# Optimization experiments

Measured on AMD Instinct MI355X. Metric: run time of the kernel, lower is better.

The kernel has to match this reference:

```python
import jax, jax.numpy as jnp
import numpy as np

N = 100000      # nodes
E = 1600000     # edges (avg degree 16)
IN = 128        # input feature dim
H = 64          # hidden size (= per-head out_channels, heads=1)
EMB = 16        # event embedding size
NEG_SLOPE = 0.2


def setup_inputs() -> dict:
    key = jax.random.key(0)
    ks = jax.random.split(key, 20)
    rn = lambda k, shape, s=0.05: jax.random.normal(k, shape, dtype=jnp.float32) * s
    inp = {
        "x": jax.random.normal(ks[0], (N, IN), dtype=jnp.float32),
        "edge_index": jax.random.randint(ks[1], (2, E), 0, N),
        "h_prev1": jax.random.normal(ks[2], (N, H), dtype=jnp.float32),
        "h_prev2": jax.random.normal(ks[3], (N, H), dtype=jnp.float32),
        # SparseGATConv params (heads=1)
        "W_gat": rn(ks[4], (H, IN)),
        "attn_l": rn(ks[5], (H,)),
        "attn_r": rn(ks[6], (H,)),
        "b_gat": jnp.zeros((H,), jnp.float32),
        # MinGRU 1
        "Wz1": rn(ks[7], (H, H)), "bz1": jnp.zeros((H,), jnp.float32),
        "Wh1": rn(ks[8], (H, H)), "bh1": jnp.zeros((H,), jnp.float32),
        # MinGRU 2
        "Wz2": rn(ks[9], (H, H)), "bz2": jnp.zeros((H,), jnp.float32),
        "Wh2": rn(ks[10], (H, H)), "bh2": jnp.zeros((H,), jnp.float32),
        # event heads
        "We1": rn(ks[11], (EMB, H)), "be1": jnp.zeros((EMB,), jnp.float32),
        "We2": rn(ks[12], (EMB, H)), "be2": jnp.zeros((EMB,), jnp.float32),
        "We3": rn(ks[13], (EMB, H)), "be3": jnp.zeros((EMB,), jnp.float32),
        # time prediction head
        "Wfc": rn(ks[14], (1, H)), "bfc": jnp.zeros((1,), jnp.float32),
    }
    return inp


def _min_gru(x, h_prev, Wz, bz, Wh, bh):
    z = jax.nn.sigmoid(x @ Wz.T + bz)
    h_tilde = jnp.tanh(x @ Wh.T + bh)
    return (1.0 - z) * h_prev + z * h_tilde


def reference(x, edge_index, h_prev1, h_prev2,
              W_gat, attn_l, attn_r, b_gat,
              Wz1, bz1, Wh1, bh1, Wz2, bz2, Wh2, bh2,
              We1, be1, We2, be2, We3, be3, Wfc, bfc):
    src, dst = edge_index[0], edge_index[1]
    # --- SparseGATConv (heads=1, concat -> [N, H]) ---
    h = x @ W_gat.T                      # [N, H]
    a1 = h @ attn_l                      # [N]  (sum over out_channels)
    a2 = h @ attn_r                      # [N]
    e = a1[src] + a2[dst]                # [E]  edge scores
    e = jnp.where(e > 0, e, NEG_SLOPE * e)  # leaky relu
    # segment softmax over incoming edges of each dst (numerically stable)
    m = jax.lax.stop_gradient(jax.ops.segment_max(e, dst, num_segments=N))
    ex = jnp.exp(e - m[dst])
    denom = jax.ops.segment_sum(ex, dst, num_segments=N)
    alpha = ex / denom[dst]              # [E]
    # dropout on alpha skipped (eval mode)
    msg = h[src] * alpha[:, None]        # [E, H]
    out = jax.ops.segment_sum(msg, dst, num_segments=N) + b_gat  # [N, H]
    # proj = Identity (gat_heads == 1)
    h1 = _min_gru(out, h_prev1, Wz1, bz1, Wh1, bh1)
    h2 = _min_gru(h1, h_prev2, Wz2, bz2, Wh2, bh2)
    c1 = h2 @ We1.T + be1
    c2 = h2 @ We2.T + be2
    c3 = h2 @ We3.T + be3
    candidate_events = jnp.stack([c1, c2, c3], axis=1)  # [N, 3, EMB]
    time_prediction = (h2 @ Wfc.T + bfc)[:, 0]          # [N]
    return candidate_events, time_prediction
```

## Files before the change

### kernel.cpp

```cpp
#include <hip/hip_runtime.h>

#define NN 100000
#define NE 1600000
#define HF 64

#define CHUNK 8192
#define NCH   196
#define NBKT  512
#define BSH   8
#define BNODES 256
#define MAXBE 5120

__device__ __forceinline__ unsigned short f2bf(float f) {
  unsigned int u = __float_as_uint(f);
  unsigned int r = (u + 0x7FFFu + ((u >> 16) & 1u)) >> 16;
  return (unsigned short)r;
}
__device__ __forceinline__ float bf2f(unsigned short s) {
  return __uint_as_float(((unsigned int)s) << 16);
}

__global__ __launch_bounds__(256) void k1_gemm_x(
    const float* __restrict__ x, const float* __restrict__ Wg,
    const float* __restrict__ attn_l, const float* __restrict__ attn_r,
    unsigned short* __restrict__ h, float* __restrict__ a1, float* __restrict__ a2)
{
  __shared__ float xa[64 * 128];
  __shared__ float wb[64 * 128];
  const int t = threadIdx.x;
  const int nbase = blockIdx.x * 64;
  const float4* Wg4 = (const float4*)Wg;
  const float4* x4  = (const float4*)x;
  float4* xa4 = (float4*)xa;
  float4* wb4 = (float4*)wb;
#pragma unroll
  for (int it = 0; it < 8; ++it) {
    int g = t + it * 256;
    int r = g >> 5, c = g & 31;
    wb4[r * 32 + (c ^ ((r >> 2) & 15))] = Wg4[g];
  }
#pragma unroll
  for (int it = 0; it < 8; ++it) {
    int g = t + it * 256;
    int r = g >> 5, c = g & 31;
    int node = nbase + r;
    float4 v = make_float4(0.f, 0.f, 0.f, 0.f);
    if (node < NN) v = x4[(size_t)node * 32 + c];
    xa4[r * 32 + (c ^ ((r >> 2) & 15))] = v;
  }
  __syncthreads();
  const int jg = t & 15, ng = t >> 4;
  const int j0 = jg * 4, n0 = ng * 4;
  float acc[4][4] = {};
#pragma unroll 8
  for (int kc = 0; kc < 32; ++kc) {
    float4 a[4], b[4];
#pragma unroll
    for (int i = 0; i < 4; ++i) a[i] = xa4[(n0 + i) * 32 + (kc ^ ng)];
#pragma unroll
    for (int j = 0; j < 4; ++j) b[j] = wb4[(j0 + j) * 32 + (kc ^ jg)];
#pragma unroll
    for (int i = 0; i < 4; ++i)
#pragma unroll
      for (int j = 0; j < 4; ++j)
        acc[i][j] += a[i].x * b[j].x + a[i].y * b[j].y + a[i].z * b[j].z + a[i].w * b[j].w;
  }
  float al[4], ar[4];
#pragma unroll
  for (int j = 0; j < 4; ++j) { al[j] = attn_l[j0 + j]; ar[j] = attn_r[j0 + j]; }
#pragma unroll
  for (int i = 0; i < 4; ++i) {
    int node = nbase + n0 + i;
    float p1 = acc[i][0]*al[0] + acc[i][1]*al[1] + acc[i][2]*al[2] + acc[i][3]*al[3];
    float p2 = acc[i][0]*ar[0] + acc[i][1]*ar[1] + acc[i][2]*ar[2] + acc[i][3]*ar[3];
#pragma unroll
    for (int m = 1; m < 16; m <<= 1) { p1 += __shfl_xor(p1, m); p2 += __shfl_xor(p2, m); }
    if (node < NN) {
      ushort4 hb;
      hb.x = f2bf(acc[i][0]); hb.y = f2bf(acc[i][1]);
      hb.z = f2bf(acc[i][2]); hb.w = f2bf(acc[i][3]);
      *(ushort4*)&h[(size_t)node * 64 + j0] = hb;
      if (jg == 0) { a1[node] = p1; a2[node] = p2; }
    }
  }
}

__global__ __launch_bounds__(256) void p1_hist(const int* __restrict__ dst,
                                               int* __restrict__ hist_blk)
{
  __shared__ int hl[NBKT];
  const int t = threadIdx.x, blk = blockIdx.x;
  for (int b = t; b < NBKT; b += 256) hl[b] = 0;
  __syncthreads();
  const int e0 = blk * CHUNK;
  const int n = min(CHUNK, NE - e0);
  for (int i = t * 4; i < n; i += 1024) {
    int4 d = *(const int4*)&dst[e0 + i];
    atomicAdd(&hl[d.x >> BSH], 1);
    atomicAdd(&hl[d.y >> BSH], 1);
    atomicAdd(&hl[d.z >> BSH], 1);
    atomicAdd(&hl[d.w >> BSH], 1);
  }
  __syncthreads();
  for (int b = t; b < NBKT; b += 256) hist_blk[blk * NBKT + b] = hl[b];
}

__global__ __launch_bounds__(256) void p2a_colscan(int* __restrict__ hist_blk,
                                                   int* __restrict__ btot)
{
  __shared__ int s[256];
  const int b = blockIdx.x, t = threadIdx.x;
  int v = (t < NCH) ? hist_blk[t * NBKT + b] : 0;
  s[t] = v;
  __syncthreads();
  for (int off = 1; off < 256; off <<= 1) {
    int add = (t >= off) ? s[t - off] : 0;
    __syncthreads();
    s[t] += add;
    __syncthreads();
  }
  if (t < NCH) hist_blk[t * NBKT + b] = s[t] - v;
  if (t == 255) btot[b] = s[255];
}

__global__ __launch_bounds__(512) void p2b_scan(const int* __restrict__ btot,
                                                int* __restrict__ bstart)
{
  __shared__ int s[512];
  const int t = threadIdx.x;
  int v = btot[t];
  s[t] = v;
  __syncthreads();
  for (int off = 1; off < 512; off <<= 1) {
    int add = (t >= off) ? s[t - off] : 0;
    __syncthreads();
    s[t] += add;
    __syncthreads();
  }
  bstart[t] = s[t] - v;
  if (t == 511) bstart[512] = s[511];
}

__global__ __launch_bounds__(256) void p3_scatter(
    const int* __restrict__ src, const int* __restrict__ dst,
    const int* __restrict__ hist_blk, const int* __restrict__ bstart,
    int2* __restrict__ part)
{
  __shared__ int hl[NBKT];
  __shared__ int loff[NBKT];
  __shared__ int cur[NBKT];
  __shared__ int sb[NBKT];
  __shared__ int q[256];
  __shared__ int2 buf[CHUNK];
  const int t = threadIdx.x, blk = blockIdx.x;
  const int e0 = blk * CHUNK;
  const int n = min(CHUNK, NE - e0);
  for (int b = t; b < NBKT; b += 256) hl[b] = 0;
  __syncthreads();
  for (int i = t * 4; i < n; i += 1024) {
    int4 d = *(const int4*)&dst[e0 + i];
    atomicAdd(&hl[d.x >> BSH], 1);
    atomicAdd(&hl[d.y >> BSH], 1);
    atomicAdd(&hl[d.z >> BSH], 1);
    atomicAdd(&hl[d.w >> BSH], 1);
  }
  __syncthreads();
  int va = hl[2 * t], vb = hl[2 * t + 1];
  int pr = va + vb;
  q[t] = pr;
  __syncthreads();
  for (int off = 1; off < 256; off <<= 1) {
    int add = (t >= off) ? q[t - off] : 0;
    __syncthreads();
    q[t] += add;
    __syncthreads();
  }
  int qe = q[t] - pr;
  loff[2 * t] = qe;       loff[2 * t + 1] = qe + va;
  cur[2 * t]  = qe;       cur[2 * t + 1]  = qe + va;
  sb[2 * t]     = bstart[2 * t]     + hist_blk[blk * NBKT + 2 * t];
  sb[2 * t + 1] = bstart[2 * t + 1] + hist_blk[blk * NBKT + 2 * t + 1];
  __syncthreads();
  for (int i = t; i < n; i += 256) {
    int s = src[e0 + i], d = dst[e0 + i];
    int p = atomicAdd(&cur[d >> BSH], 1);
    buf[p] = make_int2(s, d);
  }
  __syncthreads();
  for (int i = t; i < n; i += 256) {
    int2 e = buf[i];
    int bk = e.y >> BSH;
    part[sb[bk] + (i - loff[bk])] = e;
  }
}

__global__ __launch_bounds__(256) void p4_csr(
    const int2* __restrict__ part, const int* __restrict__ bstart,
    int* __restrict__ srcs, int* __restrict__ rs, int* __restrict__ cnt)
{
  __shared__ int cl[BNODES];
  __shared__ int s[256];
  __shared__ int rsl[BNODES];
  __shared__ int curl[BNODES];
  __shared__ int2 eb[MAXBE];
  __shared__ int osrc[MAXBE];
  const int b = blockIdx.x, t = threadIdx.x;
  const int e0 = bstart[b];
  int n = bstart[b + 1] - e0;
  if (n > MAXBE) n = MAXBE;
  cl[t] = 0;
  __syncthreads();
  for (int i = t; i < n; i += 256) {
    int2 e = part[e0 + i];
    eb[i] = e;
    atomicAdd(&cl[e.y & (BNODES - 1)], 1);
  }
  __syncthreads();
  int v = cl[t];
  s[t] = v;
  __syncthreads();
  for (int off = 1; off < 256; off <<= 1) {
    int add = (t >= off) ? s[t - off] : 0;
    __syncthreads();
    s[t] += add;
    __syncthreads();
  }
  rsl[t] = s[t] - v;
  curl[t] = s[t] - v;
  __syncthreads();
  for (int i = t; i < n; i += 256) {
    int2 e = eb[i];
    int p = atomicAdd(&curl[e.y & (BNODES - 1)], 1);
    osrc[p] = e.x;
  }
  __syncthreads();
  for (int i = t; i < n; i += 256) srcs[e0 + i] = osrc[i];
  const int node = b * BNODES + t;
  if (node < NN) { rs[node] = e0 + rsl[t]; cnt[node] = v; }
}

__global__ __launch_bounds__(256) void k5_aggregate(
    const int* __restrict__ srcs, const int* __restrict__ row_start,
    const int* __restrict__ cnt,
    const float* __restrict__ a1, const float* __restrict__ a2,
    const unsigned short* __restrict__ h, const float* __restrict__ b_gat,
    float* __restrict__ outw)
{
  const int wid  = (blockIdx.x * 256 + threadIdx.x) >> 6;
  const int lane = threadIdx.x & 63;
  if (wid >= NN) return;
  const int r0  = row_start[wid];
  const int deg = cnt[wid];
  const float a2v = a2[wid];
  const int fq = (lane & 15) * 4;
  const int eg = lane >> 4;
  float dsum = 0.f;
  float acc[4] = {0.f, 0.f, 0.f, 0.f};
  for (int base = 0; base < deg; base += 64) {
    int i = base + lane;
    int s = 0; float ex = 0.f;
    if (i < deg) {
      s = srcs[r0 + i];
      float sc = a1[s] + a2v;
      sc = sc > 0.f ? sc : 0.2f * sc;
      ex = __expf(sc);
    }
    dsum += ex;
    int nv = min(64, deg - base);
    for (int c = 0; c < nv; c += 16) {
      int se[4]; float ae[4];
#pragma unroll
      for (int u = 0; u < 4; ++u) {
        int idx = c + u * 4 + eg;
        se[u] = __shfl(s, idx);
        ae[u] = __shfl(ex, idx);
      }
      ushort4 hv[4];
#pragma unroll
      for (int u = 0; u < 4; ++u)
        hv[u] = *(const ushort4*)&h[(size_t)se[u] * 64 + fq];
#pragma unroll
      for (int u = 0; u < 4; ++u) {
        acc[0] = fmaf(ae[u], bf2f(hv[u].x), acc[0]);
        acc[1] = fmaf(ae[u], bf2f(hv[u].y), acc[1]);
        acc[2] = fmaf(ae[u], bf2f(hv[u].z), acc[2]);
        acc[3] = fmaf(ae[u], bf2f(hv[u].w), acc[3]);
      }
    }
  }
#pragma unroll
  for (int m = 1; m < 64; m <<= 1) dsum += __shfl_xor(dsum, m);
  const float inv = (deg > 0) ? 1.0f / dsum : 0.f;
#pragma unroll
  for (int k = 0; k < 4; ++k) {
    acc[k] += __shfl_xor(acc[k], 16);
    acc[k] += __shfl_xor(acc[k], 32);
  }
  if (lane < 16) {
    float4 bg = *(const float4*)&b_gat[fq];
    float4 o;
    o.x = acc[0] * inv + bg.x;
    o.y = acc[1] * inv + bg.y;
    o.z = acc[2] * inv + bg.z;
    o.w = acc[3] * inv + bg.w;
    *(float4*)&outw[(size_t)wid * 64 + fq] = o;
  }
}

__device__ __forceinline__ void stage_w64(float* dst, const float* src, int t)
{
  const float4* s4 = (const float4*)src;
  float4* d4 = (float4*)dst;
#pragma unroll
  for (int it = 0; it < 4; ++it) {
    int g = t + it * 256;
    int r = g >> 4, c = g & 15;
    d4[r * 16 + (c ^ ((r >> 2) & 15))] = s4[g];
  }
}

__device__ __forceinline__ void gemm64_acc(
    const float* at, const float* bw,
    int n0, int j0, int ng, int jg, float acc[4][4])
{
  const float4* a4 = (const float4*)at;
  const float4* b4 = (const float4*)bw;
#pragma unroll 4
  for (int kc = 0; kc < 16; ++kc) {
    float4 a[4], p[4];
#pragma unroll
    for (int i = 0; i < 4; ++i) a[i] = a4[(n0 + i) * 16 + (kc ^ ng)];
#pragma unroll
    for (int j = 0; j < 4; ++j) p[j] = b4[(j0 + j) * 16 + (kc ^ jg)];
#pragma unroll
    for (int i = 0; i < 4; ++i)
#pragma unroll
      for (int j = 0; j < 4; ++j)
        acc[i][j] += a[i].x*p[j].x + a[i].y*p[j].y + a[i].z*p[j].z + a[i].w*p[j].w;
  }
}

__device__ __forceinline__ void gru_phase(
    const float* at, const float* wz_lds, const float* wh_lds,
    const float* __restrict__ bz, const float* __restrict__ bh,
    const float* __restrict__ hp,
    int nbase, int n0, int j0, int ng, int jg, float hout[4][4])
{
  float zz[4][4];
  {
    float acc[4][4] = {};
    gemm64_acc(at, wz_lds, n0, j0, ng, jg, acc);
#pragma unroll
    for (int i = 0; i < 4; ++i)
#pragma unroll
      for (int j = 0; j < 4; ++j)
        zz[i][j] = 1.f / (1.f + __expf(-(acc[i][j] + bz[j0 + j])));
  }
  {
    float acc[4][4] = {};
    gemm64_acc(at, wh_lds, n0, j0, ng, jg, acc);
#pragma unroll
    for (int i = 0; i < 4; ++i) {
      int node = nbase + n0 + i;
      float4 hp4 = make_float4(0.f, 0.f, 0.f, 0.f);
      if (node < NN) hp4 = *(const float4*)&hp[(size_t)node * 64 + j0];
      float hpv[4] = {hp4.x, hp4.y, hp4.z, hp4.w};
#pragma unroll
      for (int j = 0; j < 4; ++j) {
        float ht = tanhf(acc[i][j] + bh[j0 + j]);
        hout[i][j] = (1.f - zz[i][j]) * hpv[j] + zz[i][j] * ht;
      }
    }
  }
}

__global__ __launch_bounds__(256) void k6_gru_heads(
    const float* __restrict__ outw,
    const float* __restrict__ hp1, const float* __restrict__ hp2,
    const float* __restrict__ Wz1, const float* __restrict__ bz1,
    const float* __restrict__ Wh1, const float* __restrict__ bh1,
    const float* __restrict__ Wz2, const float* __restrict__ bz2,
    const float* __restrict__ Wh2, const float* __restrict__ bh2,
    const float* __restrict__ We1, const float* __restrict__ We2,
    const float* __restrict__ We3, const float* __restrict__ Wfc,
    const float* __restrict__ be1, const float* __restrict__ be2,
    const float* __restrict__ be3, const float* __restrict__ bfc,
    float* __restrict__ cand, float* __restrict__ tpred)
{
  __shared__ float at[64 * 64];
  __shared__ float b1[64 * 64];
  __shared__ float b2[64 * 64];
  const int t = threadIdx.x;
  const int nbase = blockIdx.x * 64;
  const int jg = t & 15, ng = t >> 4;
  const int j0 = jg * 4, n0 = ng * 4;
  float4* at4 = (float4*)at;

  {
    const float4* o4 = (const float4*)outw;
#pragma unroll
    for (int it = 0; it < 4; ++it) {
      int g = t + it * 256;
      int r = g >> 4, c = g & 15;
      int node = nbase + r;
      float4 v = make_float4(0.f, 0.f, 0.f, 0.f);
      if (node < NN) v = o4[(size_t)node * 16 + c];
      at4[r * 16 + (c ^ ((r >> 2) & 15))] = v;
    }
  }
  stage_w64(b1, Wz1, t);
  stage_w64(b2, Wh1, t);
  __syncthreads();

  float h1v[4][4];
  gru_phase(at, b1, b2, bz1, bh1, hp1, nbase, n0, j0, ng, jg, h1v);
  __syncthreads();
#pragma unroll
  for (int i = 0; i < 4; ++i)
    at4[(n0 + i) * 16 + (jg ^ ng)] = make_float4(h1v[i][0], h1v[i][1], h1v[i][2], h1v[i][3]);
  stage_w64(b1, Wz2, t);
  stage_w64(b2, Wh2, t);
  __syncthreads();

  float h2v[4][4];
  gru_phase(at, b1, b2, bz2, bh2, hp2, nbase, n0, j0, ng, jg, h2v);
  __syncthreads();
#pragma unroll
  for (int i = 0; i < 4; ++i)
    at4[(n0 + i) * 16 + (jg ^ ng)] = make_float4(h2v[i][0], h2v[i][1], h2v[i][2], h2v[i][3]);
  {
    float4* b14 = (float4*)b1;
#pragma unroll
    for (int it = 0; it < 4; ++it) {
      int g = t + it * 256;
      int r = g >> 4, c = g & 15;
      float4 v = make_float4(0.f, 0.f, 0.f, 0.f);
      if (g < 256)       v = ((const float4*)We1)[g];
      else if (g < 512)  v = ((const float4*)We2)[g - 256];
      else if (g < 768)  v = ((const float4*)We3)[g - 512];
      else if (g < 784)  v = ((const float4*)Wfc)[g - 768];
      b14[r * 16 + (c ^ ((r >> 2) & 15))] = v;
    }
  }
  __syncthreads();

  float acc3[4][4] = {};
  gemm64_acc(at, b1, n0, j0, ng, jg, acc3);
  float bias[4];
#pragma unroll
  for (int j = 0; j < 4; ++j) {
    int jj = j0 + j;
    bias[j] = (jj < 16) ? be1[jj]
            : (jj < 32) ? be2[jj - 16]
            : (jj < 48) ? be3[jj - 32]
            : (jj == 48) ? bfc[0] : 0.f;
  }
#pragma unroll
  for (int i = 0; i < 4; ++i) {
    int node = nbase + n0 + i;
    if (node >= NN) continue;
    if (j0 < 48) {
      *(float4*)&cand[(size_t)node * 48 + j0] =
          make_float4(acc3[i][0] + bias[0], acc3[i][1] + bias[1],
                      acc3[i][2] + bias[2], acc3[i][3] + bias[3]);
    } else if (j0 == 48) {
      tpred[node] = acc3[i][0] + bias[0];
    }
  }
}

extern "C" void kernel_launch(void* const* d_in, const int* in_sizes, int n_in,
                              void* d_out, int out_size, void* d_ws, size_t ws_size,
                              hipStream_t stream)
{
  (void)in_sizes; (void)n_in; (void)out_size; (void)ws_size;
  const float* x      = (const float*)d_in[0];
  const int*   ei     = (const int*)  d_in[1];
  const float* hp1    = (const float*)d_in[2];
  const float* hp2    = (const float*)d_in[3];
  const float* Wg     = (const float*)d_in[4];
  const float* attn_l = (const float*)d_in[5];
  const float* attn_r = (const float*)d_in[6];
  const float* b_gat  = (const float*)d_in[7];
  const float* Wz1    = (const float*)d_in[8];
  const float* bz1    = (const float*)d_in[9];
  const float* Wh1    = (const float*)d_in[10];
  const float* bh1    = (const float*)d_in[11];
  const float* Wz2    = (const float*)d_in[12];
  const float* bz2    = (const float*)d_in[13];
  const float* Wh2    = (const float*)d_in[14];
  const float* bh2    = (const float*)d_in[15];
  const float* We1    = (const float*)d_in[16];
  const float* be1    = (const float*)d_in[17];
  const float* We2    = (const float*)d_in[18];
  const float* be2    = (const float*)d_in[19];
  const float* We3    = (const float*)d_in[20];
  const float* be3    = (const float*)d_in[21];
  const float* Wfc    = (const float*)d_in[22];
  const float* bfc    = (const float*)d_in[23];

  const int* srcp = ei;
  const int* dstp = ei + NE;

  char* ws = (char*)d_ws;
  unsigned short* h = (unsigned short*)(ws + 0);
  float* a1       = (float*)(ws + 12800000);
  float* a2       = (float*)(ws + 13200000);
  int*   hist_blk = (int*)  (ws + 13600000);
  int*   btot     = (int*)  (ws + 14010000);
  int*   bstart   = (int*)  (ws + 14020000);
  int*   rs       = (int*)  (ws + 14030000);
  int*   cnt      = (int*)  (ws + 14430000);
  int*   srcs     = (int*)  (ws + 14830000);
  int2*  part     = (int2*) (ws + 21230000);
  float* outw     = (float*)(ws + 21230000);

  float* cand = (float*)d_out;
  float* tp   = cand + (size_t)NN * 48;

  k1_gemm_x<<<(NN + 63) / 64, 256, 0, stream>>>(x, Wg, attn_l, attn_r, h, a1, a2);
  p1_hist<<<NCH, 256, 0, stream>>>(dstp, hist_blk);
  p2a_colscan<<<NBKT, 256, 0, stream>>>(hist_blk, btot);
  p2b_scan<<<1, 512, 0, stream>>>(btot, bstart);
  p3_scatter<<<NCH, 256, 0, stream>>>(srcp, dstp, hist_blk, bstart, part);
  p4_csr<<<(NN + BNODES - 1) / BNODES, 256, 0, stream>>>(part, bstart, srcs, rs, cnt);
  k5_aggregate<<<(NN * 64 + 255) / 256, 256, 0, stream>>>(srcs, rs, cnt, a1, a2, h, b_gat, outw);
  k6_gru_heads<<<(NN + 63) / 64, 256, 0, stream>>>(outw, hp1, hp2,
      Wz1, bz1, Wh1, bh1, Wz2, bz2, Wh2, bh2,
      We1, We2, We3, Wfc, be1, be2, be3, bfc, cand, tp);
}
```

Measured before the change: 384.1 us.

## Use bf16 MFMA for GRU and head GEMMs with bf16 aggregate output

Replaces the fp32 scalar-FMA 64x64 GEMMs in the GRU/heads kernel with bf16 MFMA 16x16x32 instructions. A small prep kernel converts and packs the weights to bf16 beforehand. The aggregation kernel now writes its output in bf16, which halves that intermediate's traffic. This trades precision on the GRU inputs and hidden states for matrix-core throughput, and adds one extra launch.

```diff
diff --git a/kernel.cpp b/kernel.cpp
--- a/kernel.cpp
+++ b/kernel.cpp
@@ -11,6 +11,9 @@
 #define BNODES 256
 #define MAXBE 5120
 
+typedef __attribute__((ext_vector_type(8))) short bf16x8;
+typedef __attribute__((ext_vector_type(4))) float f32x4;
+
 __device__ __forceinline__ unsigned short f2bf(float f) {
   unsigned int u = __float_as_uint(f);
   unsigned int r = (u + 0x7FFFu + ((u >> 16) & 1u)) >> 16;
@@ -18,6 +21,31 @@
 }
 __device__ __forceinline__ float bf2f(unsigned short s) {
   return __uint_as_float(((unsigned int)s) << 16);
+}
+
+__global__ __launch_bounds__(256) void k0_prep(
+    const float* __restrict__ Wz1, const float* __restrict__ Wh1,
+    const float* __restrict__ Wz2, const float* __restrict__ Wh2,
+    const float* __restrict__ We1, const float* __restrict__ We2,
+    const float* __restrict__ We3, const float* __restrict__ Wfc,
+    unsigned short* __restrict__ wbf)
+{
+  int idx = blockIdx.x * 256 + threadIdx.x;
+  if (idx >= 5 * 4096) return;
+  int m = idx >> 12, e = idx & 4095;
+  float v = 0.f;
+  if (m == 0) v = Wz1[e];
+  else if (m == 1) v = Wh1[e];
+  else if (m == 2) v = Wz2[e];
+  else if (m == 3) v = Wh2[e];
+  else {
+    int row = e >> 6, k = e & 63;
+    if (row < 16)      v = We1[row * 64 + k];
+    else if (row < 32) v = We2[(row - 16) * 64 + k];
+    else if (row < 48) v = We3[(row - 32) * 64 + k];
+    else if (row == 48) v = Wfc[k];
+  }
+  wbf[idx] = f2bf(v);
 }
 
 __global__ __launch_bounds__(256) void k1_gemm_x(
@@ -244,7 +272,7 @@
     const int* __restrict__ cnt,
     const float* __restrict__ a1, const float* __restrict__ a2,
     const unsigned short* __restrict__ h, const float* __restrict__ b_gat,
-    float* __restrict__ outw)
+    unsigned short* __restrict__ outw)
 {
   const int wid  = (blockIdx.x * 256 + threadIdx.x) >> 6;
   const int lane = threadIdx.x & 63;
@@ -298,173 +326,152 @@
   }
   if (lane < 16) {
     float4 bg = *(const float4*)&b_gat[fq];
-    float4 o;
-    o.x = acc[0] * inv + bg.x;
-    o.y = acc[1] * inv + bg.y;
-    o.z = acc[2] * inv + bg.z;
-    o.w = acc[3] * inv + bg.w;
-    *(float4*)&outw[(size_t)wid * 64 + fq] = o;
-  }
-}
-
-__device__ __forceinline__ void stage_w64(float* dst, const float* src, int t)
-{
-  const float4* s4 = (const float4*)src;
-  float4* d4 = (float4*)dst;
-#pragma unroll
-  for (int it = 0; it < 4; ++it) {
+    ushort4 o;
+    o.x = f2bf(acc[0] * inv + bg.x);
+    o.y = f2bf(acc[1] * inv + bg.y);
+    o.z = f2bf(acc[2] * inv + bg.z);
+    o.w = f2bf(acc[3] * inv + bg.w);
+    *(ushort4*)&outw[(size_t)wid * 64 + fq] = o;
+  }
+}
+
+__device__ __forceinline__ void stage_wb(unsigned short* dst,
+                                         const unsigned short* __restrict__ src,
+                                         int t)
+{
+#pragma unroll
+  for (int it = 0; it < 2; ++it) {
     int g = t + it * 256;
-    int r = g >> 4, c = g & 15;
-    d4[r * 16 + (c ^ ((r >> 2) & 15))] = s4[g];
-  }
-}
-
-__device__ __forceinline__ void gemm64_acc(
-    const float* at, const float* bw,
-    int n0, int j0, int ng, int jg, float acc[4][4])
-{
-  const float4* a4 = (const float4*)at;
-  const float4* b4 = (const float4*)bw;
-#pragma unroll 4
-  for (int kc = 0; kc < 16; ++kc) {
-    float4 a[4], p[4];
-#pragma unroll
-    for (int i = 0; i < 4; ++i) a[i] = a4[(n0 + i) * 16 + (kc ^ ng)];
-#pragma unroll
-    for (int j = 0; j < 4; ++j) p[j] = b4[(j0 + j) * 16 + (kc ^ jg)];
-#pragma unroll
-    for (int i = 0; i < 4; ++i)
-#pragma unroll
-      for (int j = 0; j < 4; ++j)
-        acc[i][j] += a[i].x*p[j].x + a[i].y*p[j].y + a[i].z*p[j].z + a[i].w*p[j].w;
-  }
-}
-
-__device__ __forceinline__ void gru_phase(
-    const float* at, const float* wz_lds, const float* wh_lds,
+    int r = g >> 3, c = g & 7;
+    *(bf16x8*)(dst + r * 64 + ((c ^ (r & 7)) << 3)) =
+        *(const bf16x8*)(src + (g << 3));
+  }
+}
+
+__device__ __forceinline__ void mfma_gemm_row16(
+    const unsigned short* at, const unsigned short* wl,
+    int row0, int lr, int lk, f32x4 acc[4])
+{
+#pragma unroll
+  for (int ks = 0; ks < 2; ++ks) {
+    const int ra = row0 + lr;
+    bf16x8 a = *(const bf16x8*)(at + ra * 64 + (((ks * 4 + lk) ^ (ra & 7)) << 3));
+#pragma unroll
+    for (int ct = 0; ct < 4; ++ct) {
+      const int rb = ct * 16 + lr;
+      bf16x8 b = *(const bf16x8*)(wl + rb * 64 + (((ks * 4 + lk) ^ (rb & 7)) << 3));
+      acc[ct] = __builtin_amdgcn_mfma_f32_16x16x32_bf16(a, b, acc[ct], 0, 0, 0);
+    }
+  }
+}
+
+__device__ __forceinline__ void gru_mfma(
+    const unsigned short* at, const unsigned short* wz, const unsigned short* wh,
     const float* __restrict__ bz, const float* __restrict__ bh,
     const float* __restrict__ hp,
-    int nbase, int n0, int j0, int ng, int jg, float hout[4][4])
-{
-  float zz[4][4];
-  {
-    float acc[4][4] = {};
-    gemm64_acc(at, wz_lds, n0, j0, ng, jg, acc);
-#pragma unroll
-    for (int i = 0; i < 4; ++i)
-#pragma unroll
-      for (int j = 0; j < 4; ++j)
-        zz[i][j] = 1.f / (1.f + __expf(-(acc[i][j] + bz[j0 + j])));
-  }
-  {
-    float acc[4][4] = {};
-    gemm64_acc(at, wh_lds, n0, j0, ng, jg, acc);
-#pragma unroll
-    for (int i = 0; i < 4; ++i) {
-      int node = nbase + n0 + i;
-      float4 hp4 = make_float4(0.f, 0.f, 0.f, 0.f);
-      if (node < NN) hp4 = *(const float4*)&hp[(size_t)node * 64 + j0];
-      float hpv[4] = {hp4.x, hp4.y, hp4.z, hp4.w};
-#pragma unroll
-      for (int j = 0; j < 4; ++j) {
-        float ht = tanhf(acc[i][j] + bh[j0 + j]);
-        hout[i][j] = (1.f - zz[i][j]) * hpv[j] + zz[i][j] * ht;
-      }
+    int nbase, int row0, int lr, int lk, float hv[4][4])
+{
+  f32x4 zacc[4] = {};
+  mfma_gemm_row16(at, wz, row0, lr, lk, zacc);
+  f32x4 hacc[4] = {};
+  mfma_gemm_row16(at, wh, row0, lr, lk, hacc);
+#pragma unroll
+  for (int ct = 0; ct < 4; ++ct) {
+    int j = ct * 16 + lr;
+    float bzv = bz[j], bhv = bh[j];
+#pragma unroll
+    for (int reg = 0; reg < 4; ++reg) {
+      int node = nbase + row0 + lk * 4 + reg;
+      float hpv = (node < NN) ? hp[(size_t)node * 64 + j] : 0.f;
+      float z  = 1.f / (1.f + __expf(-(zacc[ct][reg] + bzv)));
+      float ht = tanhf(hacc[ct][reg] + bhv);
+      hv[ct][reg] = (1.f - z) * hpv + z * ht;
     }
   }
 }
 
 __global__ __launch_bounds__(256) void k6_gru_heads(
-    const float* __restrict__ outw,
+    const unsigned short* __restrict__ outw,
     const float* __restrict__ hp1, const float* __restrict__ hp2,
-    const float* __restrict__ Wz1, const float* __restrict__ bz1,
-    const float* __restrict__ Wh1, const float* __restrict__ bh1,
-    const float* __restrict__ Wz2, const float* __restrict__ bz2,
-    const float* __restrict__ Wh2, const float* __restrict__ bh2,
-    const float* __restrict__ We1, const float* __restrict__ We2,
-    const float* __restrict__ We3, const float* __restrict__ Wfc,
+    const unsigned short* __restrict__ wbf,
+    const float* __restrict__ bz1, const float* __restrict__ bh1,
+    const float* __restrict__ bz2, const float* __restrict__ bh2,
     const float* __restrict__ be1, const float* __restrict__ be2,
     const float* __restrict__ be3, const float* __restrict__ bfc,
     float* __restrict__ cand, float* __restrict__ tpred)
 {
-  __shared__ float at[64 * 64];
-  __shared__ float b1[64 * 64];
-  __shared__ float b2[64 * 64];
+  __shared__ unsigned short at[64 * 64];
+  __shared__ unsigned short b1[64 * 64];
+  __shared__ unsigned short b2[64 * 64];
   const int t = threadIdx.x;
   const int nbase = blockIdx.x * 64;
-  const int jg = t & 15, ng = t >> 4;
-  const int j0 = jg * 4, n0 = ng * 4;
-  float4* at4 = (float4*)at;
-
-  {
-    const float4* o4 = (const float4*)outw;
-#pragma unroll
-    for (int it = 0; it < 4; ++it) {
-      int g = t + it * 256;
-      int r = g >> 4, c = g & 15;
-      int node = nbase + r;
-      float4 v = make_float4(0.f, 0.f, 0.f, 0.f);
-      if (node < NN) v = o4[(size_t)node * 16 + c];
-      at4[r * 16 + (c ^ ((r >> 2) & 15))] = v;
-    }
-  }
-  stage_w64(b1, Wz1, t);
-  stage_w64(b2, Wh1, t);
+  const int lane = t & 63;
+  const int w = t >> 6;
+  const int row0 = w * 16;
+  const int lr = lane & 15;
+  const int lk = lane >> 4;
+
+#pragma unroll
+  for (int it = 0; it < 2; ++it) {
+    int g = t + it * 256;
+    int r = g >> 3, c = g & 7;
+    int node = nbase + r;
+    bf16x8 v = {};
+    if (node < NN) v = *(const bf16x8*)(outw + (size_t)node * 64 + (c << 3));
+    *(bf16x8*)(at + r * 64 + ((c ^ (r & 7)) << 3)) = v;
+  }
+  stage_wb(b1, wbf + 0 * 4096, t);
+  stage_wb(b2, wbf + 1 * 4096, t);
   __syncthreads();
 
   float h1v[4][4];
-  gru_phase(at, b1, b2, bz1, bh1, hp1, nbase, n0, j0, ng, jg, h1v);
-  __syncthreads();
-#pragma unroll
-  for (int i = 0; i < 4; ++i)
-    at4[(n0 + i) * 16 + (jg ^ ng)] = make_float4(h1v[i][0], h1v[i][1], h1v[i][2], h1v[i][3]);
-  stage_w64(b1, Wz2, t);
-  stage_w64(b2, Wh2, t);
+  gru_mfma(at, b1, b2, bz1, bh1, hp1, nbase, row0, lr, lk, h1v);
+  __syncthreads();
+#pragma unroll
+  for (int ct = 0; ct < 4; ++ct)
+#pragma unroll
+    for (int reg = 0; reg < 4; ++reg) {
+      int rl = row0 + lk * 4 + reg;
+      int j = ct * 16 + lr;
+      at[rl * 64 + (((j >> 3) ^ (rl & 7)) << 3) + (j & 7)] = f2bf(h1v[ct][reg]);
+    }
+  stage_wb(b1, wbf + 2 * 4096, t);
+  stage_wb(b2, wbf + 3 * 4096, t);
   __syncthreads();
 
   float h2v[4][4];
-  gru_phase(at, b1, b2, bz2, bh2, hp2, nbase, n0, j0, ng, jg, h2v);
-  __syncthreads();
-#pragma unroll
-  for (int i = 0; i < 4; ++i)
-    at4[(n0 + i) * 16 + (jg ^ ng)] = make_float4(h2v[i][0], h2v[i][1], h2v[i][2], h2v[i][3]);
-  {
-    float4* b14 = (float4*)b1;
-#pragma unroll
-    for (int it = 0; it < 4; ++it) {
-      int g = t + it * 256;
-      int r = g >> 4, c = g & 15;
-      float4 v = make_float4(0.f, 0.f, 0.f, 0.f);
-      if (g < 256)       v = ((const float4*)We1)[g];
-      else if (g < 512)  v = ((const float4*)We2)[g - 256];
-      else if (g < 768)  v = ((const float4*)We3)[g - 512];
-      else if (g < 784)  v = ((const float4*)Wfc)[g - 768];
-      b14[r * 16 + (c ^ ((r >> 2) & 15))] = v;
-    }
-  }
-  __syncthreads();
-
-  float acc3[4][4] = {};
-  gemm64_acc(at, b1, n0, j0, ng, jg, acc3);
-  float bias[4];
-#pragma unroll
-  for (int j = 0; j < 4; ++j) {
-    int jj = j0 + j;
-    bias[j] = (jj < 16) ? be1[jj]
-            : (jj < 32) ? be2[jj - 16]
-            : (jj < 48) ? be3[jj - 32]
-            : (jj == 48) ? bfc[0] : 0.f;
-  }
-#pragma unroll
-  for (int i = 0; i < 4; ++i) {
-    int node = nbase + n0 + i;
-    if (node >= NN) continue;
-    if (j0 < 48) {
-      *(float4*)&cand[(size_t)node * 48 + j0] =
-          make_float4(acc3[i][0] + bias[0], acc3[i][1] + bias[1],
-                      acc3[i][2] + bias[2], acc3[i][3] + bias[3]);
-    } else if (j0 == 48) {
-      tpred[node] = acc3[i][0] + bias[0];
+  gru_mfma(at, b1, b2, bz2, bh2, hp2, nbase, row0, lr, lk, h2v);
+  __syncthreads();
+#pragma unroll
+  for (int ct = 0; ct < 4; ++ct)
+#pragma unroll
+    for (int reg = 0; reg < 4; ++reg) {
+      int rl = row0 + lk * 4 + reg;
+      int j = ct * 16 + lr;
+      at[rl * 64 + (((j >> 3) ^ (rl & 7)) << 3) + (j & 7)] = f2bf(h2v[ct][reg]);
+    }
+  stage_wb(b1, wbf + 4 * 4096, t);
+  __syncthreads();
+
+  f32x4 acc3[4] = {};
+  mfma_gemm_row16(at, b1, row0, lr, lk, acc3);
+#pragma unroll
+  for (int ct = 0; ct < 3; ++ct) {
+    const float* be = (ct == 0) ? be1 : (ct == 1) ? be2 : be3;
+    float bias = be[lr];
+#pragma unroll
+    for (int reg = 0; reg < 4; ++reg) {
+      int node = nbase + row0 + lk * 4 + reg;
+      if (node < NN)
+        cand[(size_t)node * 48 + ct * 16 + lr] = acc3[ct][reg] + bias;
+    }
+  }
+  if (lr == 0) {
+    float bias = bfc[0];
+#pragma unroll
+    for (int reg = 0; reg < 4; ++reg) {
+      int node = nbase + row0 + lk * 4 + reg;
+      if (node < NN) tpred[node] = acc3[3][reg] + bias;
     }
   }
 }
@@ -503,7 +510,7 @@
   const int* dstp = ei + NE;
 
   char* ws = (char*)d_ws;
-  unsigned short* h = (unsigned short*)(ws + 0);
+  unsigned short* h   = (unsigned short*)(ws + 0);
   float* a1       = (float*)(ws + 12800000);
   float* a2       = (float*)(ws + 13200000);
   int*   hist_blk = (int*)  (ws + 13600000);
@@ -513,11 +520,13 @@
   int*   cnt      = (int*)  (ws + 14430000);
   int*   srcs     = (int*)  (ws + 14830000);
   int2*  part     = (int2*) (ws + 21230000);
-  float* outw     = (float*)(ws + 21230000);
+  unsigned short* outw = (unsigned short*)(ws + 21230000);
+  unsigned short* wbf  = (unsigned short*)(ws + 34040000);
 
   float* cand = (float*)d_out;
   float* tp   = cand + (size_t)NN * 48;
 
+  k0_prep<<<80, 256, 0, stream>>>(Wz1, Wh1, Wz2, Wh2, We1, We2, We3, Wfc, wbf);
   k1_gemm_x<<<(NN + 63) / 64, 256, 0, stream>>>(x, Wg, attn_l, attn_r, h, a1, a2);
   p1_hist<<<NCH, 256, 0, stream>>>(dstp, hist_blk);
   p2a_colscan<<<NBKT, 256, 0, stream>>>(hist_blk, btot);
@@ -525,7 +534,6 @@
   p3_scatter<<<NCH, 256, 0, stream>>>(srcp, dstp, hist_blk, bstart, part);
   p4_csr<<<(NN + BNODES - 1) / BNODES, 256, 0, stream>>>(part, bstart, srcs, rs, cnt);
   k5_aggregate<<<(NN * 64 + 255) / 256, 256, 0, stream>>>(srcs, rs, cnt, a1, a2, h, b_gat, outw);
-  k6_gru_heads<<<(NN + 63) / 64, 256, 0, stream>>>(outw, hp1, hp2,
-      Wz1, bz1, Wh1, bh1, Wz2, bz2, Wh2, bh2,
-      We1, We2, We3, Wfc, be1, be2, be3, bfc, cand, tp);
-}
+  k6_gru_heads<<<(NN + 63) / 64, 256, 0, stream>>>(outw, hp1, hp2, wbf,
+      bz1, bh1, bz2, bh2, be1, be2, be3, bfc, cand, tp);
+}
```

New measurement: 331.7 us. 1.16x faster.
